# Optimization experiments

Measured on AMD Instinct MI355X. Metric: run time of the kernel, lower is better.

Reference implementation:

```python
import jax, jax.numpy as jnp
import numpy as np

QMIN, QMAX = 0.0, 255.0  # uint8 affine quantization range


def setup_inputs() -> dict:
    key = jax.random.key(0)
    ks = jax.random.split(key, 7)
    B, S, IN, OUT = 4, 2048, 4096, 4096
    x = jax.random.normal(ks[0], (B, S, IN), dtype=jnp.float32)
    weight_q = jax.random.randint(ks[1], (OUT, IN), 0, 255, dtype=jnp.int32)
    weight_scales = jax.random.uniform(ks[2], (OUT,), dtype=jnp.float32) * 0.01 + 1e-4
    weight_zero_points = jax.random.randint(ks[3], (OUT,), 0, 255, dtype=jnp.int32)
    act_scales = jax.random.uniform(ks[4], (1,), dtype=jnp.float32) * 0.05 + 1e-3
    act_zero_points = jnp.full((1,), 128, dtype=jnp.int32)
    bias = jax.random.normal(ks[5], (OUT,), dtype=jnp.float32)
    return {
        "x": x,
        "weight_q": weight_q,
        "weight_scales": weight_scales,
        "weight_zero_points": weight_zero_points,
        "act_scales": act_scales,
        "act_zero_points": act_zero_points,
        "bias": bias,
    }


def reference(x, weight_q, weight_scales, weight_zero_points, act_scales, act_zero_points, bias):
    # quantize_from_qparams on activations (per-tensor affine, uint8 range)
    a_zp = act_zero_points.astype(jnp.float32)
    x_q = jnp.clip(jnp.round(x / act_scales) + a_zp, QMIN, QMAX)
    # linear_on_quantized_data: dequantize both operands, fused matmul + bias
    x_deq = (x_q - a_zp) * act_scales  # [B, S, IN]
    w_deq = (weight_q.astype(jnp.float32) - weight_zero_points.astype(jnp.float32)[:, None]) \
            * weight_scales[:, None]  # [OUT, IN], per-output-channel scale/zp
    out = jnp.einsum("bsi,oi->bso", x_deq, w_deq) + bias  # [B, S, OUT]
    return out
```

## Files before the change

kernel.cpp:

```cpp
#include <hip/hip_runtime.h>
#include <hip/hip_bf16.h>

using int32x4 = __attribute__((ext_vector_type(4))) int;

#define BM 256
#define BN 256
#define BKB 128

#define GATE(n) asm volatile("s_waitcnt vmcnt(" #n ")" ::: "memory")

__device__ __forceinline__ void load_lds16(const void* g, void* l) {
    __builtin_amdgcn_global_load_lds(
        (const __attribute__((address_space(1))) unsigned int*)g,
        (__attribute__((address_space(3))) unsigned int*)l, 16, 0, 0);
}

__global__ __launch_bounds__(256) void quant_rows(
    const float* __restrict__ x, const float* __restrict__ act_scale,
    const int* __restrict__ act_zp, char* __restrict__ xs,
    int* __restrict__ rowsum, int K)
{
    __shared__ int wsum[4];
    const int row = blockIdx.x;
    const float s = act_scale[0];
    const int zp = act_zp[0];
    const float4* __restrict__ xr = (const float4*)(x + (size_t)row * K);
    char4* __restrict__ xo = (char4*)(xs + (size_t)row * K);
    const int nv = K >> 2;
    int sum = 0;
    for (int i = threadIdx.x; i < nv; i += 256) {
        float4 v = xr[i];
        int q0 = min(max((int)rintf(v.x / s) + zp, 0), 255) - zp;
        int q1 = min(max((int)rintf(v.y / s) + zp, 0), 255) - zp;
        int q2 = min(max((int)rintf(v.z / s) + zp, 0), 255) - zp;
        int q3 = min(max((int)rintf(v.w / s) + zp, 0), 255) - zp;
        sum += q0 + q1 + q2 + q3;
        char4 c;
        c.x = (char)q0; c.y = (char)q1; c.z = (char)q2; c.w = (char)q3;
        xo[i] = c;
    }
    for (int off = 32; off > 0; off >>= 1) sum += __shfl_down(sum, off, 64);
    if ((threadIdx.x & 63) == 0) wsum[threadIdx.x >> 6] = sum;
    __syncthreads();
    if (threadIdx.x == 0) rowsum[row] = wsum[0] + wsum[1] + wsum[2] + wsum[3];
}

__global__ __launch_bounds__(256) void wconv(
    const int4* __restrict__ wq, char4* __restrict__ wsq, long n4)
{
    long i = (long)blockIdx.x * 256 + threadIdx.x;
    if (i >= n4) return;
    int4 v = wq[i];
    char4 c;
    c.x = (char)(v.x - 128); c.y = (char)(v.y - 128);
    c.z = (char)(v.z - 128); c.w = (char)(v.w - 128);
    wsq[i] = c;
}

__global__ __launch_bounds__(256) void mkscales(
    const float* __restrict__ wscale, const int* __restrict__ wzp,
    const float* __restrict__ act_scale, float* __restrict__ alpha,
    float* __restrict__ beta, int N)
{
    int n = blockIdx.x * 256 + threadIdx.x;
    if (n >= N) return;
    float a = act_scale[0] * wscale[n];
    alpha[n] = a;
    beta[n] = a * (float)(128 - wzp[n]);
}

__global__ __launch_bounds__(512, 2) void gemm_i8(
    const char* __restrict__ Aq, const char* __restrict__ Bq,
    const int* __restrict__ rowsum, const float* __restrict__ alpha,
    const float* __restrict__ beta, const float* __restrict__ bias,
    float* __restrict__ C, int M, int N, int K)
{
    __shared__ __align__(16) char As[2][BM * BKB];
    __shared__ __align__(16) char Bs[2][BN * BKB];

    const int tid = threadIdx.x;
    const int w   = tid >> 6;
    const int l   = tid & 63;

    const int nwg = gridDim.x;
    const int nbx = N / BN;
    const int orig = blockIdx.x;
    const int xcd = orig & 7;
    const int rest = orig >> 3;
    const int qq = nwg >> 3, rr = nwg & 7;
    const int wg = (xcd < rr ? xcd * (qq + 1) : rr * (qq + 1) + (xcd - rr) * qq)
                   + rest;
    const int n0 = (wg % nbx) * BN;
    const int m0 = (wg / nbx) * BM;

    const int wm = (w & 1) * 128;
    const int wn = (w >> 1) * 64;

    const int lr8 = l >> 3;
    const int csw = (((l & 7) ^ (lr8 & 7)) << 4);
    const int rB0 = w * 16;
    const int rA2 = (w < 4) ? (w * 16) : (128 + (w - 4) * 16);

    const char* sB0 = Bq + (size_t)(n0 + rB0 + lr8) * K + csw;
    const char* sB1 = sB0 + (size_t)128 * K;
    const char* sA2 = Aq + (size_t)(m0 + rA2 + lr8) * K + csw;
    const char* sA3 = sA2 + (size_t)64 * K;
    const size_t k8 = (size_t)8 * K;

    const int oB0 = rB0 * BKB;
    const int oB1 = oB0 + 128 * BKB;
    const int oA2 = rA2 * BKB;
    const int oA3 = oA2 + 64 * BKB;

    const int r   = l & 15;
    const int qk  = l >> 4;
    const int rx  = r & 7;
    const int rof = r * BKB;
    const int ck0 = ((qk ^ rx) << 4);
    const int ck1 = (((4 + qk) ^ rx) << 4);

    int32x4 acc[8][4] = {};
    const int NT = K / BKB;

    load_lds16(sB0,      Bs[0] + oB0);
    load_lds16(sB0 + k8, Bs[0] + oB0 + 1024);
    load_lds16(sB1,      Bs[0] + oB1);
    load_lds16(sB1 + k8, Bs[0] + oB1 + 1024);
    load_lds16(sA2,      As[0] + oA2);
    load_lds16(sA2 + k8, As[0] + oA2 + 1024);
    load_lds16(sA3,      As[0] + oA3);
    load_lds16(sA3 + k8, As[0] + oA3 + 1024);
    sB0 += BKB; sB1 += BKB; sA2 += BKB; sA3 += BKB;

    int s = 0;
    for (int T = 0; T < NT; ++T) {
        const char* cA = As[s];
        const char* cB = Bs[s];
        char* nA = As[s ^ 1];
        char* nB = Bs[s ^ 1];
        const bool stage = (T + 1 < NT);
        int32x4 bf[4][2];
#pragma unroll
        for (int p = 0; p < 4; ++p) {
            if (p == 0) { GATE(2); }
            if (p == 2) { if (stage) { GATE(4); } else { GATE(0); } }
            __builtin_amdgcn_s_barrier();

            int32x4 af[2][2];
            const char* ab = cA + (wm + p * 32) * BKB + rof;
            af[0][0] = *(const int32x4*)(ab + ck0);
            af[0][1] = *(const int32x4*)(ab + ck1);
            af[1][0] = *(const int32x4*)(ab + 2048 + ck0);
            af[1][1] = *(const int32x4*)(ab + 2048 + ck1);
            if (p == 0) {
                const char* bb = cB + wn * BKB + rof;
#pragma unroll
                for (int j = 0; j < 4; ++j) {
                    bf[j][0] = *(const int32x4*)(bb + j * 2048 + ck0);
                    bf[j][1] = *(const int32x4*)(bb + j * 2048 + ck1);
                }
            }
            if (stage) {
                if (p == 0) { load_lds16(sB0, nB + oB0);
                              load_lds16(sB0 + k8, nB + oB0 + 1024); }
                if (p == 1) { load_lds16(sB1, nB + oB1);
                              load_lds16(sB1 + k8, nB + oB1 + 1024); }
                if (p == 2) { load_lds16(sA2, nA + oA2);
                              load_lds16(sA2 + k8, nA + oA2 + 1024); }
                if (p == 3) { load_lds16(sA3, nA + oA3);
                              load_lds16(sA3 + k8, nA + oA3 + 1024); }
            }
            asm volatile("s_waitcnt lgkmcnt(0)" ::: "memory");
            __builtin_amdgcn_sched_barrier(0);
            __builtin_amdgcn_s_setprio(1);
#pragma unroll
            for (int i = 0; i < 2; ++i)
#pragma unroll
                for (int j = 0; j < 4; ++j) {
                    acc[p * 2 + i][j] = __builtin_amdgcn_mfma_i32_16x16x64_i8(
                        af[i][0], bf[j][0], acc[p * 2 + i][j], 0, 0, 0);
                    acc[p * 2 + i][j] = __builtin_amdgcn_mfma_i32_16x16x64_i8(
                        af[i][1], bf[j][1], acc[p * 2 + i][j], 0, 0, 0);
                }
            __builtin_amdgcn_s_setprio(0);
        }
        sB0 += BKB; sB1 += BKB; sA2 += BKB; sA3 += BKB;
        s ^= 1;
    }

    const int r4  = qk * 4;
    const int cil = r;
#pragma unroll
    for (int j = 0; j < 4; ++j) {
        const int col = n0 + wn + j * 16 + cil;
        const float al = alpha[col];
        const float be = beta[col];
        const float bi = bias[col];
#pragma unroll
        for (int mi = 0; mi < 8; ++mi) {
            const int rowb = m0 + wm + mi * 16 + r4;
#pragma unroll
            for (int t = 0; t < 4; ++t) {
                const int row = rowb + t;
                C[(size_t)row * N + col] =
                    al * (float)acc[mi][j][t] + be * (float)rowsum[row] + bi;
            }
        }
    }
}

extern "C" void kernel_launch(void* const* d_in, const int* in_sizes, int n_in,
                              void* d_out, int out_size, void* d_ws, size_t ws_size,
                              hipStream_t stream) {
    const float* x      = (const float*)d_in[0];
    const int*   wq     = (const int*)d_in[1];
    const float* wscale = (const float*)d_in[2];
    const int*   wzp    = (const int*)d_in[3];
    const float* ascale = (const float*)d_in[4];
    const int*   azp    = (const int*)d_in[5];
    const float* bias   = (const float*)d_in[6];
    float* out = (float*)d_out;

    const int N = in_sizes[2];
    const int K = in_sizes[1] / N;
    const int M = in_sizes[0] / K;

    char* ws     = (char*)d_ws;
    char* xs     = ws;
    char* wsq    = ws + (size_t)M * K;
    int*  rowsum = (int*)(wsq + (size_t)N * K);
    float* alpha = (float*)((char*)rowsum + (size_t)M * 4);
    float* beta  = (float*)((char*)alpha + (size_t)N * 4);

    quant_rows<<<M, 256, 0, stream>>>(x, ascale, azp, xs, rowsum, K);

    long n4 = (long)N * K / 4;
    wconv<<<(int)((n4 + 255) / 256), 256, 0, stream>>>(
        (const int4*)wq, (char4*)wsq, n4);

    mkscales<<<(N + 255) / 256, 256, 0, stream>>>(wscale, wzp, ascale, alpha, beta, N);

    dim3 grid((M / BM) * (N / BN));
    gemm_i8<<<grid, 512, 0, stream>>>(xs, wsq, rowsum, alpha, beta, bias, out, M, N, K);
}
```

Measured before the change: 426.0 us.

## Merge prep kernels, fold scale computation into epilogue, prefetch B two tiles ahead

Three prep launches (activation quantization, weight conversion, scale computation) become one merged launch, and alpha and beta are now computed inline in the GEMM epilogue. The GEMM pipeline is reworked so B tiles are prefetched two K-steps ahead into a reused buffer, while A loads are issued all at once at phase 0. This cuts launch overhead and aims to hide more global-load latency, but the LDS reuse for B and the new vmcnt gates carry ordering hazards.

```diff
diff --git a/kernel.cpp b/kernel.cpp
--- a/kernel.cpp
+++ b/kernel.cpp
@@ -15,65 +15,53 @@
         (__attribute__((address_space(3))) unsigned int*)l, 16, 0, 0);
 }
 
-__global__ __launch_bounds__(256) void quant_rows(
+__global__ __launch_bounds__(256) void prep(
     const float* __restrict__ x, const float* __restrict__ act_scale,
     const int* __restrict__ act_zp, char* __restrict__ xs,
-    int* __restrict__ rowsum, int K)
-{
-    __shared__ int wsum[4];
-    const int row = blockIdx.x;
-    const float s = act_scale[0];
-    const int zp = act_zp[0];
-    const float4* __restrict__ xr = (const float4*)(x + (size_t)row * K);
-    char4* __restrict__ xo = (char4*)(xs + (size_t)row * K);
-    const int nv = K >> 2;
-    int sum = 0;
-    for (int i = threadIdx.x; i < nv; i += 256) {
-        float4 v = xr[i];
-        int q0 = min(max((int)rintf(v.x / s) + zp, 0), 255) - zp;
-        int q1 = min(max((int)rintf(v.y / s) + zp, 0), 255) - zp;
-        int q2 = min(max((int)rintf(v.z / s) + zp, 0), 255) - zp;
-        int q3 = min(max((int)rintf(v.w / s) + zp, 0), 255) - zp;
-        sum += q0 + q1 + q2 + q3;
-        char4 c;
-        c.x = (char)q0; c.y = (char)q1; c.z = (char)q2; c.w = (char)q3;
-        xo[i] = c;
-    }
-    for (int off = 32; off > 0; off >>= 1) sum += __shfl_down(sum, off, 64);
-    if ((threadIdx.x & 63) == 0) wsum[threadIdx.x >> 6] = sum;
-    __syncthreads();
-    if (threadIdx.x == 0) rowsum[row] = wsum[0] + wsum[1] + wsum[2] + wsum[3];
-}
-
-__global__ __launch_bounds__(256) void wconv(
+    int* __restrict__ rowsum, int K, int M,
     const int4* __restrict__ wq, char4* __restrict__ wsq, long n4)
 {
-    long i = (long)blockIdx.x * 256 + threadIdx.x;
-    if (i >= n4) return;
-    int4 v = wq[i];
-    char4 c;
-    c.x = (char)(v.x - 128); c.y = (char)(v.y - 128);
-    c.z = (char)(v.z - 128); c.w = (char)(v.w - 128);
-    wsq[i] = c;
-}
-
-__global__ __launch_bounds__(256) void mkscales(
-    const float* __restrict__ wscale, const int* __restrict__ wzp,
-    const float* __restrict__ act_scale, float* __restrict__ alpha,
-    float* __restrict__ beta, int N)
-{
-    int n = blockIdx.x * 256 + threadIdx.x;
-    if (n >= N) return;
-    float a = act_scale[0] * wscale[n];
-    alpha[n] = a;
-    beta[n] = a * (float)(128 - wzp[n]);
+    if (blockIdx.x < (unsigned)M) {
+        __shared__ int wsum[4];
+        const int row = blockIdx.x;
+        const float s = act_scale[0];
+        const int zp = act_zp[0];
+        const float4* __restrict__ xr = (const float4*)(x + (size_t)row * K);
+        char4* __restrict__ xo = (char4*)(xs + (size_t)row * K);
+        const int nv = K >> 2;
+        int sum = 0;
+        for (int i = threadIdx.x; i < nv; i += 256) {
+            float4 v = xr[i];
+            int q0 = min(max((int)rintf(v.x / s) + zp, 0), 255) - zp;
+            int q1 = min(max((int)rintf(v.y / s) + zp, 0), 255) - zp;
+            int q2 = min(max((int)rintf(v.z / s) + zp, 0), 255) - zp;
+            int q3 = min(max((int)rintf(v.w / s) + zp, 0), 255) - zp;
+            sum += q0 + q1 + q2 + q3;
+            char4 c;
+            c.x = (char)q0; c.y = (char)q1; c.z = (char)q2; c.w = (char)q3;
+            xo[i] = c;
+        }
+        for (int off = 32; off > 0; off >>= 1) sum += __shfl_down(sum, off, 64);
+        if ((threadIdx.x & 63) == 0) wsum[threadIdx.x >> 6] = sum;
+        __syncthreads();
+        if (threadIdx.x == 0) rowsum[row] = wsum[0] + wsum[1] + wsum[2] + wsum[3];
+    } else {
+        long i = (long)(blockIdx.x - M) * 256 + threadIdx.x;
+        if (i >= n4) return;
+        int4 v = wq[i];
+        char4 c;
+        c.x = (char)(v.x - 128); c.y = (char)(v.y - 128);
+        c.z = (char)(v.z - 128); c.w = (char)(v.w - 128);
+        wsq[i] = c;
+    }
 }
 
 __global__ __launch_bounds__(512, 2) void gemm_i8(
     const char* __restrict__ Aq, const char* __restrict__ Bq,
-    const int* __restrict__ rowsum, const float* __restrict__ alpha,
-    const float* __restrict__ beta, const float* __restrict__ bias,
-    float* __restrict__ C, int M, int N, int K)
+    const int* __restrict__ rowsum, const float* __restrict__ wscale,
+    const int* __restrict__ wzp, const float* __restrict__ ascale,
+    const float* __restrict__ bias, float* __restrict__ C,
+    int M, int N, int K)
 {
     __shared__ __align__(16) char As[2][BM * BKB];
     __shared__ __align__(16) char Bs[2][BN * BKB];
@@ -130,20 +118,28 @@
     load_lds16(sA2 + k8, As[0] + oA2 + 1024);
     load_lds16(sA3,      As[0] + oA3);
     load_lds16(sA3 + k8, As[0] + oA3 + 1024);
-    sB0 += BKB; sB1 += BKB; sA2 += BKB; sA3 += BKB;
+    if (NT > 1) {
+        load_lds16(sB0 + BKB,      Bs[1] + oB0);
+        load_lds16(sB0 + BKB + k8, Bs[1] + oB0 + 1024);
+        load_lds16(sB1 + BKB,      Bs[1] + oB1);
+        load_lds16(sB1 + BKB + k8, Bs[1] + oB1 + 1024);
+    }
+    sA2 += BKB; sA3 += BKB;
+    sB0 += 2 * (size_t)BKB; sB1 += 2 * (size_t)BKB;
 
     int s = 0;
     for (int T = 0; T < NT; ++T) {
         const char* cA = As[s];
         const char* cB = Bs[s];
         char* nA = As[s ^ 1];
-        char* nB = Bs[s ^ 1];
-        const bool stage = (T + 1 < NT);
+        char* nB = Bs[s];
+        const bool stA = (T + 1 < NT);
+        const bool stB = (T + 2 < NT);
         int32x4 bf[4][2];
 #pragma unroll
         for (int p = 0; p < 4; ++p) {
-            if (p == 0) { GATE(2); }
-            if (p == 2) { if (stage) { GATE(4); } else { GATE(0); } }
+            if (p == 0) { if (stA) { GATE(6); } else { GATE(2); } }
+            if (p == 2) { if (stA) { GATE(8); } else { GATE(0); } }
             __builtin_amdgcn_s_barrier();
 
             int32x4 af[2][2];
@@ -159,16 +155,18 @@
                     bf[j][0] = *(const int32x4*)(bb + j * 2048 + ck0);
                     bf[j][1] = *(const int32x4*)(bb + j * 2048 + ck1);
                 }
+                if (stA) {
+                    load_lds16(sA2,      nA + oA2);
+                    load_lds16(sA2 + k8, nA + oA2 + 1024);
+                    load_lds16(sA3,      nA + oA3);
+                    load_lds16(sA3 + k8, nA + oA3 + 1024);
+                }
             }
-            if (stage) {
-                if (p == 0) { load_lds16(sB0, nB + oB0);
-                              load_lds16(sB0 + k8, nB + oB0 + 1024); }
-                if (p == 1) { load_lds16(sB1, nB + oB1);
-                              load_lds16(sB1 + k8, nB + oB1 + 1024); }
-                if (p == 2) { load_lds16(sA2, nA + oA2);
-                              load_lds16(sA2 + k8, nA + oA2 + 1024); }
-                if (p == 3) { load_lds16(sA3, nA + oA3);
-                              load_lds16(sA3 + k8, nA + oA3 + 1024); }
+            if (p == 2 && stB) {
+                load_lds16(sB0,      nB + oB0);
+                load_lds16(sB0 + k8, nB + oB0 + 1024);
+                load_lds16(sB1,      nB + oB1);
+                load_lds16(sB1 + k8, nB + oB1 + 1024);
             }
             asm volatile("s_waitcnt lgkmcnt(0)" ::: "memory");
             __builtin_amdgcn_sched_barrier(0);
@@ -184,17 +182,18 @@
                 }
             __builtin_amdgcn_s_setprio(0);
         }
-        sB0 += BKB; sB1 += BKB; sA2 += BKB; sA3 += BKB;
+        sA2 += BKB; sA3 += BKB; sB0 += BKB; sB1 += BKB;
         s ^= 1;
     }
 
+    const float as = ascale[0];
     const int r4  = qk * 4;
     const int cil = r;
 #pragma unroll
     for (int j = 0; j < 4; ++j) {
         const int col = n0 + wn + j * 16 + cil;
-        const float al = alpha[col];
-        const float be = beta[col];
+        const float al = as * wscale[col];
+        const float be = al * (float)(128 - wzp[col]);
         const float bi = bias[col];
 #pragma unroll
         for (int mi = 0; mi < 8; ++mi) {
@@ -229,17 +228,13 @@
     char* xs     = ws;
     char* wsq    = ws + (size_t)M * K;
     int*  rowsum = (int*)(wsq + (size_t)N * K);
-    float* alpha = (float*)((char*)rowsum + (size_t)M * 4);
-    float* beta  = (float*)((char*)alpha + (size_t)N * 4);
-
-    quant_rows<<<M, 256, 0, stream>>>(x, ascale, azp, xs, rowsum, K);
 
     long n4 = (long)N * K / 4;
-    wconv<<<(int)((n4 + 255) / 256), 256, 0, stream>>>(
-        (const int4*)wq, (char4*)wsq, n4);
-
-    mkscales<<<(N + 255) / 256, 256, 0, stream>>>(wscale, wzp, ascale, alpha, beta, N);
+    int wblocks = (int)((n4 + 255) / 256);
+    prep<<<M + wblocks, 256, 0, stream>>>(
+        x, ascale, azp, xs, rowsum, K, M, (const int4*)wq, (char4*)wsq, n4);
 
     dim3 grid((M / BM) * (N / BN));
-    gemm_i8<<<grid, 512, 0, stream>>>(xs, wsq, rowsum, alpha, beta, bias, out, M, N, K);
-}
+    gemm_i8<<<grid, 512, 0, stream>>>(
+        xs, wsq, rowsum, wscale, wzp, ascale, bias, out, M, N, K);
+}
```

Measured after the change: 413.9 us. 1.03x faster.
